# Kernel optimization log

Measured on AMD Instinct MI355X. Metric: run time of the kernel, lower is better.

The kernel has to match this reference:

```python
import jax, jax.numpy as jnp
import numpy as np

N = 262144   # total atoms/nodes in the batch
F = 128      # node feature dim
G = 4096     # number of graphs (segments)
H = 512      # n_hidden
T = 3        # set2set recurrent steps


def hard_sigmoid(x):
    return jnp.clip(0.2 * x + 0.5, 0.0, 1.0)


def setup_inputs() -> dict:
    key = jax.random.key(0)
    k1, k2, k3, k4 = jax.random.split(key, 4)
    features = jax.random.normal(k1, (1, N, F), dtype=jnp.float32)
    weights = jax.random.uniform(k2, (1, N), dtype=jnp.float32)
    # sorted graph ids, every segment non-empty (TF segment_* need sorted ids)
    index = ((jnp.arange(N) * G) // N).astype(jnp.int32).reshape(1, N)
    m_weight = jax.random.normal(k3, (F, H), dtype=jnp.float32) * 0.05
    m_bias = jnp.zeros((H,), dtype=jnp.float32)
    recurrent_kernel = jax.random.normal(k4, (2 * H, 4 * H), dtype=jnp.float32) * 0.02
    # unit_forget_bias: [zeros(H), ones(H), zeros(2H)]
    recurrent_bias = jnp.concatenate(
        [jnp.zeros((H,)), jnp.ones((H,)), jnp.zeros((2 * H,))]).astype(jnp.float32)
    return {
        "features": features,
        "weights": weights,
        "index": index,
        "m_weight": m_weight,
        "m_bias": m_bias,
        "recurrent_kernel": recurrent_kernel,
        "recurrent_bias": recurrent_bias,
    }


def reference(features, weights, index, m_weight, m_bias,
              recurrent_kernel, recurrent_bias):
    idx = index.reshape(-1)                       # [N]
    m = features @ m_weight + m_bias              # [1, N, H]
    c = jnp.zeros((1, G, H), dtype=features.dtype)
    q_star = jnp.zeros((1, G, 2 * H), dtype=features.dtype)
    for _ in range(T):
        # LSTM cell on q_star
        z = q_star @ recurrent_kernel + recurrent_bias   # [1, G, 4H]
        zi, zf, zc, zo = jnp.split(z, 4, axis=-1)
        i = hard_sigmoid(zi)
        f = hard_sigmoid(zf)
        c = f * c + i * jnp.tanh(zc)
        h = hard_sigmoid(zo) * jnp.tanh(c)               # [1, G, H]
        # per-node attention logits
        h_nodes = h[:, idx, :]                           # [1, N, H] gather
        e = jnp.sum(m * h_nodes, axis=-1)                # [1, N]
        maxes = jax.ops.segment_max(e[0], idx, num_segments=G,
                                    indices_are_sorted=True)
        e = e - maxes[idx][None, :]
        ex = jnp.exp(e) * weights                        # weighted softmax numerator
        seg_sum = jax.ops.segment_sum(ex[0], idx, num_segments=G,
                                      indices_are_sorted=True)
        a = ex / seg_sum[idx][None, :]                   # [1, N]
        r = jax.ops.segment_sum((m * a[..., None])[0], idx, num_segments=G,
                                indices_are_sorted=True)[None]  # [1, G, H]
        q_star = jnp.concatenate([h, r], axis=-1)        # [1, G, 2H]
    return q_star
```

## Files before the change

### kernel.cpp

```cpp
#include <hip/hip_runtime.h>
#include <cstddef>

#define NN 262144
#define F_DIM 128
#define G_SEG 4096
#define H_DIM 512
#define SEG_SZ 64
#define KDIM 1024
#define NDIM 2048
#define KA 640

typedef unsigned short u16;
typedef __attribute__((ext_vector_type(8))) __bf16 bf16x8;
typedef __attribute__((ext_vector_type(4))) float f32x4;

__device__ __forceinline__ float hsig(float x) {
    return fminf(fmaxf(0.2f * x + 0.5f, 0.0f), 1.0f);
}

__device__ __forceinline__ u16 f2bf(float x) {
    union { float f; unsigned u; } v; v.f = x;
    unsigned r = (v.u + 0x7fffu + ((v.u >> 16) & 1u)) >> 16;
    return (u16)r;
}

__global__ void k_transpose(const float* __restrict__ mw, float* __restrict__ mwT) {
    int id = blockIdx.x * blockDim.x + threadIdx.x;
    if (id < F_DIM * H_DIM) {
        int f = id / H_DIM, j = id % H_DIM;
        mwT[j * F_DIM + f] = mw[id];
    }
}

__device__ __forceinline__ int permrow(int n) {
    int q = n >> 9, jj = n & 511;
    return (jj >> 5) * 128 + q * 32 + (jj & 31);
}

__global__ __launch_bounds__(256) void k_bt(const float* __restrict__ rk, u16* __restrict__ btg2) {
    __shared__ u16 t[64][65];
    int tid = threadIdx.x;
    int n0 = blockIdx.x * 64, k0 = blockIdx.y * 64;
    for (int i = tid; i < 64 * 64; i += 256) {
        int r = i >> 6, cc = i & 63;
        t[r][cc] = f2bf(rk[(size_t)(k0 + r) * NDIM + n0 + cc]);
    }
    __syncthreads();
    for (int i = tid; i < 64 * 64; i += 256) {
        int n = i >> 6, k = i & 63;
        btg2[(size_t)permrow(n0 + n) * KA + k0 + k] = t[k][n];
    }
}

__global__ __launch_bounds__(256) void k_M2(const float* __restrict__ rk,
                                            const float* __restrict__ mwT,
                                            u16* __restrict__ btg2) {
    __shared__ float srk[64][64];
    __shared__ float smw[64][128];
    int n0 = blockIdx.x * 64;
    int t = threadIdx.x;
    int f = t & 127, nh = t >> 7;
    float acc[32] = {};
    for (int k0 = 0; k0 < H_DIM; k0 += 64) {
        for (int i = t; i < 64 * 64; i += 256) {
            int kk = i >> 6, nn = i & 63;
            srk[kk][nn] = rk[(size_t)(512 + k0 + kk) * NDIM + n0 + nn];
        }
        for (int i = t; i < 64 * 128; i += 256) {
            int ff = i & 127, kk = i >> 7;
            smw[kk][ff] = mwT[(size_t)(k0 + kk) * F_DIM + ff];
        }
        __syncthreads();
        for (int kk = 0; kk < 64; ++kk) {
            float w = smw[kk][f];
#pragma unroll
            for (int s = 0; s < 32; ++s)
                acc[s] = fmaf(w, srk[kk][nh * 32 + s], acc[s]);
        }
        __syncthreads();
    }
    for (int s = 0; s < 32; ++s) {
        int n = n0 + nh * 32 + s;
        btg2[(size_t)permrow(n) * KA + 512 + f] = f2bf(acc[s]);
    }
}

__global__ __launch_bounds__(256) void k_rb2(const float* __restrict__ rk,
                                             const float* __restrict__ rb,
                                             const float* __restrict__ mb,
                                             float* __restrict__ rb2) {
    int n = blockIdx.x * 256 + threadIdx.x;
    float acc = rb[n];
    for (int j = 0; j < H_DIM; ++j)
        acc = fmaf(mb[j], rk[(size_t)(512 + j) * NDIM + n], acc);
    rb2[n] = acc;
}

#define GBM 128
#define GBK 32
__global__ __launch_bounds__(256) void k_gemm_gates(const u16* __restrict__ A,
                                                    const u16* __restrict__ BTG,
                                                    const float* __restrict__ rb2,
                                                    float* __restrict__ c,
                                                    float* __restrict__ out,
                                                    u16* __restrict__ qsa) {
    __shared__ u16 sA[GBM * GBK];
    __shared__ u16 sB[GBM * GBK];
    int tid = threadIdx.x;
    int lane = tid & 63, wv = tid >> 6;
    int wm = wv * 32;
    int bm = blockIdx.y * GBM;
    int j0 = blockIdx.x * 32;
    const u16* Ab = A + (size_t)bm * KA;
    const u16* Bb = BTG + (size_t)(blockIdx.x * 128) * KA;
    int r16 = lane & 15, kc = lane >> 4;
    f32x4 acc[2][8] = {};

    for (int k0 = 0; k0 < KA; k0 += GBK) {
#pragma unroll
        for (int i = 0; i < 2; ++i) {
            int ch = i * 256 + tid;
            int row = ch >> 2, cc = ch & 3;
            int ccs = cc ^ ((row >> 1) & 3);
            __builtin_amdgcn_global_load_lds(
                (const __attribute__((address_space(1))) void*)(Ab + (size_t)row * KA + k0 + ccs * 8),
                (__attribute__((address_space(3))) void*)(&sA[ch * 8]), 16, 0, 0);
            __builtin_amdgcn_global_load_lds(
                (const __attribute__((address_space(1))) void*)(Bb + (size_t)row * KA + k0 + ccs * 8),
                (__attribute__((address_space(3))) void*)(&sB[ch * 8]), 16, 0, 0);
        }
        __syncthreads();
        bf16x8 af[2], bfr[8];
#pragma unroll
        for (int mi = 0; mi < 2; ++mi) {
            int row = wm + mi * 16 + r16;
            int off = row * GBK + ((kc ^ ((row >> 1) & 3)) * 8);
            af[mi] = *reinterpret_cast<const bf16x8*>(&sA[off]);
        }
#pragma unroll
        for (int ni = 0; ni < 8; ++ni) {
            int row = ni * 16 + r16;
            int off = row * GBK + ((kc ^ ((row >> 1) & 3)) * 8);
            bfr[ni] = *reinterpret_cast<const bf16x8*>(&sB[off]);
        }
#pragma unroll
        for (int mi = 0; mi < 2; ++mi)
#pragma unroll
            for (int ni = 0; ni < 8; ++ni)
                acc[mi][ni] = __builtin_amdgcn_mfma_f32_16x16x32_bf16(af[mi], bfr[ni], acc[mi][ni], 0, 0, 0);
        __syncthreads();
    }

    float rbv[4][2];
#pragma unroll
    for (int q = 0; q < 4; ++q) {
        rbv[q][0] = rb2[q * H_DIM + j0 + r16];
        rbv[q][1] = rb2[q * H_DIM + j0 + 16 + r16];
    }
#pragma unroll
    for (int mi = 0; mi < 2; ++mi)
#pragma unroll
        for (int r = 0; r < 4; ++r) {
            int row = bm + wm + mi * 16 + kc * 4 + r;
#pragma unroll
            for (int jj = 0; jj < 2; ++jj) {
                int j = j0 + jj * 16 + r16;
                float zi = acc[mi][0 + jj][r] + rbv[0][jj];
                float zf = acc[mi][2 + jj][r] + rbv[1][jj];
                float zc = acc[mi][4 + jj][r] + rbv[2][jj];
                float zo = acc[mi][6 + jj][r] + rbv[3][jj];
                size_t ci = (size_t)row * H_DIM + j;
                float cn = hsig(zf) * c[ci] + hsig(zi) * tanhf(zc);
                c[ci] = cn;
                float h = hsig(zo) * tanhf(cn);
                out[(size_t)row * 1024 + j] = h;
                qsa[(size_t)row * KA + j] = f2bf(h);
            }
        }
}

__global__ void k_gates0(const float* __restrict__ rb,
                         float* __restrict__ c, float* __restrict__ out,
                         u16* __restrict__ qsa) {
    int id = blockIdx.x * blockDim.x + threadIdx.x;
    int g = id >> 9, j = id & 511;
    float zi = rb[j], zc = rb[2 * H_DIM + j], zo = rb[3 * H_DIM + j];
    float cn = hsig(zi) * tanhf(zc);
    c[id] = cn;
    float h = hsig(zo) * tanhf(cn);
    out[(size_t)g * 1024 + j] = h;
    qsa[(size_t)g * KA + j] = f2bf(h);
}

#define WSEG 16
__global__ __launch_bounds__(256) void k_W(const float* __restrict__ out,
                                           const float* __restrict__ mwT,
                                           const float* __restrict__ mb,
                                           float* __restrict__ W,
                                           float* __restrict__ bsum) {
    __shared__ float smw[128][F_DIM];
    __shared__ float shl[WSEG][128];
    __shared__ float smb[128];
    __shared__ float bacc[WSEG][16];
    int g0 = blockIdx.x * WSEG;
    int t = threadIdx.x;
    int f = t & 127, sh = t >> 7;
    bacc[t >> 4][t & 15] = 0.f;
    float acc[8] = {};
    for (int k0 = 0; k0 < H_DIM; k0 += 128) {
        for (int i = t; i < 128 * 32; i += 256) {
            int r = i >> 5, c4 = (i & 31) << 2;
            *reinterpret_cast<float4*>(&smw[r][c4]) =
                *reinterpret_cast<const float4*>(&mwT[(size_t)(k0 + r) * F_DIM + c4]);
        }
        for (int i = t; i < WSEG * 32; i += 256) {
            int s = i >> 5, c4 = (i & 31) << 2;
            *reinterpret_cast<float4*>(&shl[s][c4]) =
                *reinterpret_cast<const float4*>(&out[(size_t)(g0 + s) * 1024 + k0 + c4]);
        }
        if (t < 128) smb[t] = mb[k0 + t];
        __syncthreads();
        for (int kk = 0; kk < 128; ++kk) {
            float w = smw[kk][f];
#pragma unroll
            for (int s = 0; s < 8; ++s)
                acc[s] = fmaf(shl[sh + 2 * s][kk], w, acc[s]);
        }
        {
            int s = t >> 4, l16 = t & 15;
            float pb = 0.f;
#pragma unroll
            for (int m = 0; m < 8; ++m)
                pb = fmaf(shl[s][l16 * 8 + m], smb[l16 * 8 + m], pb);
            bacc[s][l16] += pb;
        }
        __syncthreads();
    }
#pragma unroll
    for (int s = 0; s < 8; ++s)
        W[(size_t)(g0 + sh + 2 * s) * F_DIM + f] = acc[s];
    if (t < WSEG) {
        float b = 0.f;
#pragma unroll
        for (int i = 0; i < 16; ++i) b += bacc[t][i];
        bsum[g0 + t] = b;
    }
}

__global__ __launch_bounds__(128) void k_attn(const float* __restrict__ feats,
                                              const float* __restrict__ wts,
                                              const float* __restrict__ W,
                                              const float* __restrict__ bsum,
                                              float* __restrict__ fsum,
                                              u16* __restrict__ qsa,
                                              int gmul) {
    int g = blockIdx.x;
    int t = threadIdx.x;
    __shared__ float fl[SEG_SZ * 129];
    __shared__ float Wl[F_DIM];
    __shared__ float ep[2][SEG_SZ];
    __shared__ float al[SEG_SZ];
    const float4* f4 = reinterpret_cast<const float4*>(feats + (size_t)g * SEG_SZ * F_DIM);
    for (int i = t; i < SEG_SZ * F_DIM / 4; i += 128) {
        float4 v = f4[i];
        int n = i >> 5;
        int f = (i & 31) << 2;
        float* p = &fl[n * 129 + f];
        p[0] = v.x; p[1] = v.y; p[2] = v.z; p[3] = v.w;
    }
    Wl[t] = W[(size_t)(g * gmul) * F_DIM + t];
    __syncthreads();
    int row = t & 63, half = t >> 6;
    const float* fr = &fl[row * 129 + half * 64];
    const float* wr = &Wl[half * 64];
    float e = 0.f;
#pragma unroll
    for (int f = 0; f < 64; ++f) e = fmaf(fr[f], wr[f], e);
    ep[half][row] = e;
    __syncthreads();
    if (t < 64) {
        float ee = ep[0][t] + ep[1][t] + bsum[g * gmul];
        float mx = ee;
#pragma unroll
        for (int off = 32; off >= 1; off >>= 1) mx = fmaxf(mx, __shfl_xor(mx, off));
        float ex = expf(ee - mx) * wts[g * SEG_SZ + t];
        float s = ex;
#pragma unroll
        for (int off = 32; off >= 1; off >>= 1) s += __shfl_xor(s, off);
        al[t] = ex / s;
    }
    __syncthreads();
    float a0 = 0.f;
#pragma unroll
    for (int n = 0; n < SEG_SZ; ++n)
        a0 = fmaf(al[n], fl[n * 129 + t], a0);
    fsum[g * F_DIM + t] = a0;
    qsa[(size_t)g * KA + 512 + t] = f2bf(a0);
}

#define RGB 8
__global__ __launch_bounds__(512) void k_r(const float* __restrict__ fsum,
                                           const float* __restrict__ mw,
                                           const float* __restrict__ mb,
                                           float* __restrict__ out) {
    int g0 = blockIdx.x * RGB;
    int tid = threadIdx.x;
    __shared__ float fs[RGB][F_DIM];
    for (int i = tid; i < RGB * F_DIM; i += 512)
        fs[i >> 7][i & 127] = fsum[g0 * F_DIM + i];
    __syncthreads();
    float acc[RGB] = {};
    for (int f = 0; f < F_DIM; ++f) {
        float w = mw[f * H_DIM + tid];
#pragma unroll
        for (int s = 0; s < RGB; ++s) acc[s] = fmaf(fs[s][f], w, acc[s]);
    }
    float bias = mb[tid];
#pragma unroll
    for (int s = 0; s < RGB; ++s)
        out[(size_t)(g0 + s) * 1024 + H_DIM + tid] = acc[s] + bias;
}

extern "C" void kernel_launch(void* const* d_in, const int* in_sizes, int n_in,
                              void* d_out, int out_size, void* d_ws, size_t ws_size,
                              hipStream_t stream) {
    const float* feats = (const float*)d_in[0];
    const float* wts   = (const float*)d_in[1];
    const float* mw    = (const float*)d_in[3];
    const float* mb    = (const float*)d_in[4];
    const float* rk    = (const float*)d_in[5];
    const float* rb    = (const float*)d_in[6];
    float* out = (float*)d_out;

    float* c    = (float*)d_ws;
    float* W    = c + (size_t)G_SEG * H_DIM;
    float* bs   = W + (size_t)G_SEG * F_DIM;
    float* fsum = bs + G_SEG;
    float* mwT  = fsum + (size_t)G_SEG * F_DIM;
    float* rb2  = mwT + (size_t)H_DIM * F_DIM;
    u16*   qsa  = (u16*)(rb2 + NDIM);
    u16*   btg2 = qsa + (size_t)G_SEG * KA;

    k_transpose<<<(F_DIM * H_DIM + 255) / 256, 256, 0, stream>>>(mw, mwT);
    k_bt<<<dim3(NDIM / 64, 512 / 64), 256, 0, stream>>>(rk, btg2);
    k_M2<<<NDIM / 64, 256, 0, stream>>>(rk, mwT, btg2);
    k_rb2<<<NDIM / 256, 256, 0, stream>>>(rk, rb, mb, rb2);

    for (int t = 0; t < 3; ++t) {
        if (t > 0) {
            k_gemm_gates<<<dim3(H_DIM / 32, G_SEG / GBM), 256, 0, stream>>>(qsa, btg2, rb2, c, out, qsa);
        } else {
            k_gates0<<<(G_SEG * H_DIM) / 256, 256, 0, stream>>>(rb, c, out, qsa);
        }
        k_W<<<(t == 0) ? 1 : (G_SEG / WSEG), 256, 0, stream>>>(out, mwT, mb, W, bs);
        k_attn<<<G_SEG, 128, 0, stream>>>(feats, wts, W, bs, fsum, qsa, (t == 0) ? 0 : 1);
        if (t == 2)
            k_r<<<G_SEG / RGB, 512, 0, stream>>>(fsum, mw, mb, out);
    }
}
```

Before: 551.4 us.

## Double-buffer gate GEMM LDS tiles and split-K weight precompute with atomics

The gate GEMM now double-buffers its LDS tiles, so each next K-slice is fetched while the MFMAs run on the current one. Because the GEMM reads qsa while it writes h into the same buffer, ping-pong q buffers are added to remove that read/write race. The setup kernels k_M2 and k_rb2 are split along K across more blocks and combined with float atomicAdd, which needs memsets and a separate bf16 conversion pass. This trades more launches and nondeterministic summation order for more parallelism in setup and overlapped loads in the GEMM.

```diff
diff --git a/kernel.cpp b/kernel.cpp
--- a/kernel.cpp
+++ b/kernel.cpp
@@ -54,35 +54,39 @@
 
 __global__ __launch_bounds__(256) void k_M2(const float* __restrict__ rk,
                                             const float* __restrict__ mwT,
-                                            u16* __restrict__ btg2) {
-    __shared__ float srk[64][64];
-    __shared__ float smw[64][128];
-    int n0 = blockIdx.x * 64;
+                                            float* __restrict__ M2f) {
+    __shared__ float smw[128][F_DIM];
+    __shared__ float srk[128][32];
+    int n0 = blockIdx.x * 32, k0 = blockIdx.y * 128;
     int t = threadIdx.x;
-    int f = t & 127, nh = t >> 7;
-    float acc[32] = {};
-    for (int k0 = 0; k0 < H_DIM; k0 += 64) {
-        for (int i = t; i < 64 * 64; i += 256) {
-            int kk = i >> 6, nn = i & 63;
-            srk[kk][nn] = rk[(size_t)(512 + k0 + kk) * NDIM + n0 + nn];
-        }
-        for (int i = t; i < 64 * 128; i += 256) {
-            int ff = i & 127, kk = i >> 7;
-            smw[kk][ff] = mwT[(size_t)(k0 + kk) * F_DIM + ff];
-        }
-        __syncthreads();
-        for (int kk = 0; kk < 64; ++kk) {
-            float w = smw[kk][f];
-#pragma unroll
-            for (int s = 0; s < 32; ++s)
-                acc[s] = fmaf(w, srk[kk][nh * 32 + s], acc[s]);
-        }
-        __syncthreads();
-    }
-    for (int s = 0; s < 32; ++s) {
-        int n = n0 + nh * 32 + s;
-        btg2[(size_t)permrow(n) * KA + 512 + f] = f2bf(acc[s]);
-    }
+    for (int i = t; i < 128 * 32; i += 256) {
+        int r = i >> 5, c4 = (i & 31) << 2;
+        *reinterpret_cast<float4*>(&smw[r][c4]) =
+            *reinterpret_cast<const float4*>(&mwT[(size_t)(k0 + r) * F_DIM + c4]);
+    }
+    for (int i = t; i < 128 * 32; i += 256) {
+        int kk = i >> 5, nn = i & 31;
+        srk[kk][nn] = rk[(size_t)(512 + k0 + kk) * NDIM + n0 + nn];
+    }
+    __syncthreads();
+    int f = t & 127, h = t >> 7;
+    float acc[16] = {};
+    for (int kk = 0; kk < 128; ++kk) {
+        float w = smw[kk][f];
+#pragma unroll
+        for (int s = 0; s < 16; ++s)
+            acc[s] = fmaf(w, srk[kk][h * 16 + s], acc[s]);
+    }
+#pragma unroll
+    for (int s = 0; s < 16; ++s)
+        atomicAdd(&M2f[(size_t)f * NDIM + n0 + h * 16 + s], acc[s]);
+}
+
+__global__ __launch_bounds__(256) void k_M2cvt(const float* __restrict__ M2f,
+                                               u16* __restrict__ btg2) {
+    int id = blockIdx.x * 256 + threadIdx.x;
+    int f = id >> 11, n = id & 2047;
+    btg2[(size_t)permrow(n) * KA + 512 + f] = f2bf(M2f[id]);
 }
 
 __global__ __launch_bounds__(256) void k_rb2(const float* __restrict__ rk,
@@ -90,22 +94,24 @@
                                              const float* __restrict__ mb,
                                              float* __restrict__ rb2) {
     int n = blockIdx.x * 256 + threadIdx.x;
-    float acc = rb[n];
-    for (int j = 0; j < H_DIM; ++j)
-        acc = fmaf(mb[j], rk[(size_t)(512 + j) * NDIM + n], acc);
-    rb2[n] = acc;
+    int j0 = blockIdx.y * 128;
+    float acc = (blockIdx.y == 0) ? rb[n] : 0.f;
+    for (int j = 0; j < 128; ++j)
+        acc = fmaf(mb[j0 + j], rk[(size_t)(512 + j0 + j) * NDIM + n], acc);
+    atomicAdd(&rb2[n], acc);
 }
 
 #define GBM 128
 #define GBK 32
+#define NKT (KA / GBK)
 __global__ __launch_bounds__(256) void k_gemm_gates(const u16* __restrict__ A,
                                                     const u16* __restrict__ BTG,
                                                     const float* __restrict__ rb2,
                                                     float* __restrict__ c,
                                                     float* __restrict__ out,
-                                                    u16* __restrict__ qsa) {
-    __shared__ u16 sA[GBM * GBK];
-    __shared__ u16 sB[GBM * GBK];
+                                                    u16* __restrict__ qout) {
+    __shared__ u16 sA[2][GBM * GBK];
+    __shared__ u16 sB[2][GBM * GBK];
     int tid = threadIdx.x;
     int lane = tid & 63, wv = tid >> 6;
     int wm = wv * 32;
@@ -116,32 +122,57 @@
     int r16 = lane & 15, kc = lane >> 4;
     f32x4 acc[2][8] = {};
 
-    for (int k0 = 0; k0 < KA; k0 += GBK) {
-#pragma unroll
-        for (int i = 0; i < 2; ++i) {
-            int ch = i * 256 + tid;
-            int row = ch >> 2, cc = ch & 3;
-            int ccs = cc ^ ((row >> 1) & 3);
+    int srow = tid >> 2, scc = tid & 3;
+    int sccs = scc ^ ((srow >> 1) & 3);
+    int srow2 = (256 + tid) >> 2, scc2 = tid & 3;
+    int sccs2 = scc2 ^ ((srow2 >> 1) & 3);
+
+    {
+        __builtin_amdgcn_global_load_lds(
+            (const __attribute__((address_space(1))) void*)(Ab + (size_t)srow * KA + sccs * 8),
+            (__attribute__((address_space(3))) void*)(&sA[0][tid * 8]), 16, 0, 0);
+        __builtin_amdgcn_global_load_lds(
+            (const __attribute__((address_space(1))) void*)(Bb + (size_t)srow * KA + sccs * 8),
+            (__attribute__((address_space(3))) void*)(&sB[0][tid * 8]), 16, 0, 0);
+        __builtin_amdgcn_global_load_lds(
+            (const __attribute__((address_space(1))) void*)(Ab + (size_t)srow2 * KA + sccs2 * 8),
+            (__attribute__((address_space(3))) void*)(&sA[0][(256 + tid) * 8]), 16, 0, 0);
+        __builtin_amdgcn_global_load_lds(
+            (const __attribute__((address_space(1))) void*)(Bb + (size_t)srow2 * KA + sccs2 * 8),
+            (__attribute__((address_space(3))) void*)(&sB[0][(256 + tid) * 8]), 16, 0, 0);
+    }
+    __syncthreads();
+
+    for (int kt = 0; kt < NKT; ++kt) {
+        int cur = kt & 1;
+        if (kt < NKT - 1) {
+            int k0n = (kt + 1) * GBK;
+            int nxt = cur ^ 1;
             __builtin_amdgcn_global_load_lds(
-                (const __attribute__((address_space(1))) void*)(Ab + (size_t)row * KA + k0 + ccs * 8),
-                (__attribute__((address_space(3))) void*)(&sA[ch * 8]), 16, 0, 0);
+                (const __attribute__((address_space(1))) void*)(Ab + (size_t)srow * KA + k0n + sccs * 8),
+                (__attribute__((address_space(3))) void*)(&sA[nxt][tid * 8]), 16, 0, 0);
             __builtin_amdgcn_global_load_lds(
-                (const __attribute__((address_space(1))) void*)(Bb + (size_t)row * KA + k0 + ccs * 8),
-                (__attribute__((address_space(3))) void*)(&sB[ch * 8]), 16, 0, 0);
-        }
-        __syncthreads();
+                (const __attribute__((address_space(1))) void*)(Bb + (size_t)srow * KA + k0n + sccs * 8),
+                (__attribute__((address_space(3))) void*)(&sB[nxt][tid * 8]), 16, 0, 0);
+            __builtin_amdgcn_global_load_lds(
+                (const __attribute__((address_space(1))) void*)(Ab + (size_t)srow2 * KA + k0n + sccs2 * 8),
+                (__attribute__((address_space(3))) void*)(&sA[nxt][(256 + tid) * 8]), 16, 0, 0);
+            __builtin_amdgcn_global_load_lds(
+                (const __attribute__((address_space(1))) void*)(Bb + (size_t)srow2 * KA + k0n + sccs2 * 8),
+                (__attribute__((address_space(3))) void*)(&sB[nxt][(256 + tid) * 8]), 16, 0, 0);
+        }
         bf16x8 af[2], bfr[8];
 #pragma unroll
         for (int mi = 0; mi < 2; ++mi) {
             int row = wm + mi * 16 + r16;
             int off = row * GBK + ((kc ^ ((row >> 1) & 3)) * 8);
-            af[mi] = *reinterpret_cast<const bf16x8*>(&sA[off]);
+            af[mi] = *reinterpret_cast<const bf16x8*>(&sA[cur][off]);
         }
 #pragma unroll
         for (int ni = 0; ni < 8; ++ni) {
             int row = ni * 16 + r16;
             int off = row * GBK + ((kc ^ ((row >> 1) & 3)) * 8);
-            bfr[ni] = *reinterpret_cast<const bf16x8*>(&sB[off]);
+            bfr[ni] = *reinterpret_cast<const bf16x8*>(&sB[cur][off]);
         }
 #pragma unroll
         for (int mi = 0; mi < 2; ++mi)
@@ -174,14 +205,14 @@
                 c[ci] = cn;
                 float h = hsig(zo) * tanhf(cn);
                 out[(size_t)row * 1024 + j] = h;
-                qsa[(size_t)row * KA + j] = f2bf(h);
+                qout[(size_t)row * KA + j] = f2bf(h);
             }
         }
 }
 
 __global__ void k_gates0(const float* __restrict__ rb,
                          float* __restrict__ c, float* __restrict__ out,
-                         u16* __restrict__ qsa) {
+                         u16* __restrict__ qout) {
     int id = blockIdx.x * blockDim.x + threadIdx.x;
     int g = id >> 9, j = id & 511;
     float zi = rb[j], zc = rb[2 * H_DIM + j], zo = rb[3 * H_DIM + j];
@@ -189,7 +220,7 @@
     c[id] = cn;
     float h = hsig(zo) * tanhf(cn);
     out[(size_t)g * 1024 + j] = h;
-    qsa[(size_t)g * KA + j] = f2bf(h);
+    qout[(size_t)g * KA + j] = f2bf(h);
 }
 
 #define WSEG 16
@@ -252,7 +283,7 @@
                                               const float* __restrict__ W,
                                               const float* __restrict__ bsum,
                                               float* __restrict__ fsum,
-                                              u16* __restrict__ qsa,
+                                              u16* __restrict__ qout,
                                               int gmul) {
     int g = blockIdx.x;
     int t = threadIdx.x;
@@ -295,7 +326,7 @@
     for (int n = 0; n < SEG_SZ; ++n)
         a0 = fmaf(al[n], fl[n * 129 + t], a0);
     fsum[g * F_DIM + t] = a0;
-    qsa[(size_t)g * KA + 512 + t] = f2bf(a0);
+    qout[(size_t)g * KA + 512 + t] = f2bf(a0);
 }
 
 #define RGB 8
@@ -338,22 +369,30 @@
     float* fsum = bs + G_SEG;
     float* mwT  = fsum + (size_t)G_SEG * F_DIM;
     float* rb2  = mwT + (size_t)H_DIM * F_DIM;
-    u16*   qsa  = (u16*)(rb2 + NDIM);
-    u16*   btg2 = qsa + (size_t)G_SEG * KA;
-
+    float* M2f  = rb2 + NDIM;
+    u16*   qsa0 = (u16*)(M2f + (size_t)F_DIM * NDIM);
+    u16*   qsa1 = qsa0 + (size_t)G_SEG * KA;
+    u16*   btg2 = qsa1 + (size_t)G_SEG * KA;
+
+    hipMemsetAsync(rb2, 0, NDIM * sizeof(float), stream);
+    hipMemsetAsync(M2f, 0, (size_t)F_DIM * NDIM * sizeof(float), stream);
     k_transpose<<<(F_DIM * H_DIM + 255) / 256, 256, 0, stream>>>(mw, mwT);
     k_bt<<<dim3(NDIM / 64, 512 / 64), 256, 0, stream>>>(rk, btg2);
-    k_M2<<<NDIM / 64, 256, 0, stream>>>(rk, mwT, btg2);
-    k_rb2<<<NDIM / 256, 256, 0, stream>>>(rk, rb, mb, rb2);
-
+    k_M2<<<dim3(NDIM / 32, 4), 256, 0, stream>>>(rk, mwT, M2f);
+    k_M2cvt<<<(F_DIM * NDIM) / 256, 256, 0, stream>>>(M2f, btg2);
+    k_rb2<<<dim3(NDIM / 256, 4), 256, 0, stream>>>(rk, rb, mb, rb2);
+
+    u16* qbuf[2] = {qsa0, qsa1};
     for (int t = 0; t < 3; ++t) {
+        u16* qin  = qbuf[t & 1];
+        u16* qout = qbuf[(t + 1) & 1];
         if (t > 0) {
-            k_gemm_gates<<<dim3(H_DIM / 32, G_SEG / GBM), 256, 0, stream>>>(qsa, btg2, rb2, c, out, qsa);
+            k_gemm_gates<<<dim3(H_DIM / 32, G_SEG / GBM), 256, 0, stream>>>(qin, btg2, rb2, c, out, qout);
         } else {
-            k_gates0<<<(G_SEG * H_DIM) / 256, 256, 0, stream>>>(rb, c, out, qsa);
+            k_gates0<<<(G_SEG * H_DIM) / 256, 256, 0, stream>>>(rb, c, out, qout);
         }
         k_W<<<(t == 0) ? 1 : (G_SEG / WSEG), 256, 0, stream>>>(out, mwT, mb, W, bs);
-        k_attn<<<G_SEG, 128, 0, stream>>>(feats, wts, W, bs, fsum, qsa, (t == 0) ? 0 : 1);
+        k_attn<<<G_SEG, 128, 0, stream>>>(feats, wts, W, bs, fsum, qout, (t == 0) ? 0 : 1);
         if (t == 2)
             k_r<<<G_SEG / RGB, 512, 0, stream>>>(fsum, mw, mb, out);
     }
```

Result: no change. 546.4 us (-0.9%).
